# Kernel optimization log

Hardware: AMD Instinct MI355X
Metric: run time of the kernel (lower is better)

Reference implementation:

```python
import jax, jax.numpy as jnp
import numpy as np

H = 56; W = 56; WS = 7; SS = 3; NH = 12; DIM = 384; B = 32
N = WS * WS                      # 49 tokens per window
NW = (H // WS) * (W // WS)       # 64 windows per image
HID = 4 * DIM
EPS = 1e-5


def _rel_index():
    coords = np.stack(np.meshgrid(np.arange(WS), np.arange(WS), indexing='ij'))  # [2,ws,ws]
    cf = coords.reshape(2, -1)
    rel = (cf[:, :, None] - cf[:, None, :]).transpose(1, 2, 0)  # [N,N,2]
    rel[..., 0] += WS - 1
    rel[..., 1] += WS - 1
    rel[..., 0] *= 2 * WS - 1
    return rel.sum(-1).astype(np.int32)  # [N,N] in [0,169)


def _attn_mask():
    img = np.zeros((H, W), np.float32)
    cnt = 0
    sl = (slice(0, -WS), slice(-WS, -SS), slice(-SS, None))
    for h in sl:
        for w in sl:
            img[h, w] = cnt
            cnt += 1
    mw = img.reshape(H // WS, WS, W // WS, WS).transpose(0, 2, 1, 3).reshape(-1, N)  # [nW,N]
    am = mw[:, None, :] - mw[:, :, None]  # [nW,N,N]
    return np.where(am != 0, np.float32(-100.0), np.float32(0.0)).astype(np.float32)


def _ln(x, g, b):
    m = jnp.mean(x, axis=-1, keepdims=True)
    v = jnp.mean(jnp.square(x - m), axis=-1, keepdims=True)
    return (x - m) * jax.lax.rsqrt(v + EPS) * g + b


def setup_inputs() -> dict:
    key = jax.random.key(0)
    ks = jax.random.split(key, 8)
    s = 0.02
    return {
        'x': jax.random.normal(ks[0], (B, H * W, DIM), jnp.float32),
        'qkv_w': jax.random.normal(ks[1], (3 * DIM, DIM), jnp.float32) * s,
        'qkv_b': jnp.zeros((3 * DIM,), jnp.float32),
        'proj_w': jax.random.normal(ks[2], (DIM, DIM), jnp.float32) * s,
        'proj_b': jnp.zeros((DIM,), jnp.float32),
        'rpb_table': jax.random.normal(ks[3], ((2 * WS - 1) ** 2, NH), jnp.float32) * s,
        'ln1_g': jnp.ones((DIM,), jnp.float32),
        'ln1_b': jnp.zeros((DIM,), jnp.float32),
        'fc1_w': jax.random.normal(ks[4], (HID, DIM), jnp.float32) * s,
        'fc1_b': jnp.zeros((HID,), jnp.float32),
        'fc2_w': jax.random.normal(ks[5], (DIM, HID), jnp.float32) * s,
        'fc2_b': jnp.zeros((DIM,), jnp.float32),
        'ln2_g': jnp.ones((DIM,), jnp.float32),
        'ln2_b': jnp.zeros((DIM,), jnp.float32),
        'attn_mask': jnp.asarray(_attn_mask()),
        'rel_idx': jnp.asarray(_rel_index()),
    }


def reference(x, qkv_w, qkv_b, proj_w, proj_b, rpb_table, ln1_g, ln1_b,
              fc1_w, fc1_b, fc2_w, fc2_b, ln2_g, ln2_b, attn_mask, rel_idx):
    Bb, L, C = x.shape
    hd = C // NH
    scale = hd ** -0.5
    shortcut = x
    # cyclic shift
    xs = jnp.roll(x.reshape(Bb, H, W, C), (-SS, -SS), axis=(1, 2))
    # window partition -> [Bb*nW, N, C]
    xw = xs.reshape(Bb, H // WS, WS, W // WS, WS, C).transpose(0, 1, 3, 2, 4, 5).reshape(-1, N, C)
    # qkv
    qkv = (xw @ qkv_w.T + qkv_b).reshape(-1, N, 3, NH, hd).transpose(2, 0, 3, 1, 4)
    q, k, v = qkv[0] * scale, qkv[1], qkv[2]          # [Bb*nW, NH, N, hd]
    attn = jnp.einsum('whnd,whmd->whnm', q, k)        # [Bb*nW, NH, N, N]
    bias = rpb_table[rel_idx.reshape(-1)].reshape(N, N, NH).transpose(2, 0, 1)
    attn = attn + bias[None]
    # shifted-window mask
    attn = attn.reshape(Bb, NW, NH, N, N) + attn_mask[None, :, None]
    attn = jax.nn.softmax(attn.reshape(-1, NH, N, N), axis=-1)
    out = jnp.einsum('whnm,whmd->whnd', attn, v).transpose(0, 2, 1, 3).reshape(-1, N, C)
    out = out @ proj_w.T + proj_b
    # window reverse + roll back
    xs = out.reshape(Bb, H // WS, W // WS, WS, WS, C).transpose(0, 1, 3, 2, 4, 5).reshape(Bb, H, W, C)
    xs = jnp.roll(xs, (SS, SS), axis=(1, 2)).reshape(Bb, L, C)
    # post-norm residuals (as in source: shortcut + norm(attn_out); x += norm(ffn(x)))
    x1 = shortcut + _ln(xs, ln1_g, ln1_b)
    y = jax.nn.gelu(x1 @ fc1_w.T + fc1_b, approximate=False) @ fc2_w.T + fc2_b
    return x1 + _ln(y, ln2_g, ln2_b)
```

## Files before the change

### kernel.cpp

```cpp
#include <hip/hip_runtime.h>
#include <hip/hip_bf16.h>
#include <math.h>

typedef __hip_bfloat16 bf16;
typedef __bf16 bf16x8 __attribute__((ext_vector_type(8)));
typedef float f32x4 __attribute__((ext_vector_type(4)));

#define HH 56
#define WW 56
#define WSZ 7
#define SSH 3
#define NHEAD 12
#define CDIM 384
#define BBATCH 32
#define NTOK 49
#define NWIN 64
#define HIDD 1536
#define HD 32
#define NWTOT (BBATCH*NWIN)
#define MROWS (NWTOT*NTOK)
#define MHALF (MROWS/2)
#define LTOT (HH*WW)
#define EPSLN 1e-5f
#define QSCALE 0.17677669529663687f
#define NEGBIG -1e30f

enum { M_QK = 0, M_V = 1, M_FC1 = 2 };

__device__ __forceinline__ void gload16(const void* g, void* l) {
    __builtin_amdgcn_global_load_lds(
        (const __attribute__((address_space(1))) void*)g,
        (__attribute__((address_space(3))) void*)l, 16, 0, 0);
}

__device__ __forceinline__ unsigned short bfbits(float v) {
    bf16 b = __float2bfloat16(v);
    return *reinterpret_cast<unsigned short*>(&b);
}

__device__ __forceinline__ int xcd_swz(int orig, int nwg) {
    const int q = nwg >> 3, r = nwg & 7;
    const int xcd = orig & 7, loc = orig >> 3;
    return (xcd < r ? xcd * (q + 1) : r * (q + 1) + (xcd - r) * q) + loc;
}

__global__ __launch_bounds__(256) void cvt_k(const float* __restrict__ src,
                                             bf16* __restrict__ dst, int n) {
    int i = blockIdx.x * 256 + threadIdx.x;
    if (i < n) dst[i] = __float2bfloat16(src[i]);
}

__global__ __launch_bounds__(256)
void tbl_k(const float* __restrict__ rpb, const int* __restrict__ relidx,
           const float* __restrict__ amask, float* __restrict__ tbl) {
    int idx = blockIdx.x * 256 + threadIdx.x;
    int m = idx & 63, n = (idx >> 6) & 63;
    int h = (idx >> 12) % NHEAD, wi = idx / (64 * 64 * NHEAD);
    float v;
    if (m >= NTOK) v = NEGBIG;
    else if (n >= NTOK) v = 0.f;
    else v = rpb[relidx[n * NTOK + m] * NHEAD + h] + amask[((long)wi * NTOK + n) * NTOK + m];
    tbl[idx] = v;
}

__global__ __launch_bounds__(256) void gather_k(const float* __restrict__ x,
                                                bf16* __restrict__ xw) {
    int idx = blockIdx.x * 256 + threadIdx.x;
    int rr = idx / 96, c4 = (idx % 96) * 4;
    int w = rr / 49, ti = rr % 49;
    int b = w >> 6, wi = w & 63;
    int hy = (wi >> 3) * 7 + ti / 7;
    int hx = (wi & 7) * 7 + ti % 7;
    int sh = hy + SSH; if (sh >= HH) sh -= HH;
    int sw = hx + SSH; if (sw >= WW) sw -= WW;
    float4 v = *(const float4*)&x[((long)b * LTOT + sh * WW + sw) * CDIM + c4];
    bf16* o = &xw[(long)rr * CDIM + c4];
    o[0] = __float2bfloat16(v.x); o[1] = __float2bfloat16(v.y);
    o[2] = __float2bfloat16(v.z); o[3] = __float2bfloat16(v.w);
}

template<int MODE, int KDIM, int NTN>
__global__ __launch_bounds__(256)
void mgemm_k(const bf16* __restrict__ A, const bf16* __restrict__ Wt,
             const float* __restrict__ bias, void* __restrict__ Outp)
{
    constexpr bool SWAP = (MODE != M_V);
    __shared__ bf16 As[2][128 * 64];
    __shared__ bf16 Bs[2][128 * 64];
    const int tid = threadIdx.x;
    const int wid = tid >> 6, lane = tid & 63;

    const int gid = xcd_swz(blockIdx.x, gridDim.x);
    const int m0 = (gid / NTN) * 128;
    const int n0 = (gid % NTN) * 128;

    const int srow = lane >> 3, sseg = lane & 7;
    const int swseg = sseg ^ (srow & 7);
    const bf16* Ag = A + (long)(m0 + wid * 32 + srow) * KDIM + swseg * 8;
    const bf16* Wg = Wt + (long)(n0 + wid * 32 + srow) * KDIM + swseg * 8;

    const int wr = (wid >> 1) * 64, wc = (wid & 1) * 64;
    const int l15 = lane & 15, g4 = lane >> 4;

    f32x4 acc[4][4] = {};

    auto STAGE = [&](int b, int t) {
#pragma unroll
        for (int i = 0; i < 4; ++i) {
            gload16(Ag + (long)(i * 8) * KDIM + t * 64, &As[b][(wid * 32 + i * 8) * 64]);
            gload16(Wg + (long)(i * 8) * KDIM + t * 64, &Bs[b][(wid * 32 + i * 8) * 64]);
        }
    };

    const int nt = KDIM / 64;
    STAGE(0, 0);
    STAGE(1, 1);
    asm volatile("s_waitcnt vmcnt(8)" ::: "memory");
    __builtin_amdgcn_s_barrier();

    int buf = 0;
    for (int t = 0; t < nt; ++t) {
        bf16x8 af[2][4], bfr[2][4];
#pragma unroll
        for (int kk = 0; kk < 2; ++kk)
#pragma unroll
            for (int i = 0; i < 4; ++i) {
                const int ra = wr + i * 16 + l15;
                const int rb = wc + i * 16 + l15;
                const int sa = (4 * kk + g4) ^ (ra & 7);
                const int sb = (4 * kk + g4) ^ (rb & 7);
                af[kk][i]  = *(const bf16x8*)&As[buf][ra * 64 + sa * 8];
                bfr[kk][i] = *(const bf16x8*)&Bs[buf][rb * 64 + sb * 8];
            }
        __builtin_amdgcn_sched_barrier(0);
        asm volatile("s_waitcnt lgkmcnt(0)" ::: "memory");
        __builtin_amdgcn_sched_barrier(0);
        __builtin_amdgcn_s_barrier();
        if (t + 2 < nt) STAGE(buf, t + 2);
#pragma unroll
        for (int kk = 0; kk < 2; ++kk)
#pragma unroll
            for (int mi = 0; mi < 4; ++mi)
#pragma unroll
                for (int ni = 0; ni < 4; ++ni) {
                    if (SWAP)
                        acc[ni][mi] = __builtin_amdgcn_mfma_f32_16x16x32_bf16(
                            bfr[kk][ni], af[kk][mi], acc[ni][mi], 0, 0, 0);
                    else
                        acc[mi][ni] = __builtin_amdgcn_mfma_f32_16x16x32_bf16(
                            af[kk][mi], bfr[kk][ni], acc[mi][ni], 0, 0, 0);
                }
        if (t + 2 < nt) { asm volatile("s_waitcnt vmcnt(8)" ::: "memory"); }
        else            { asm volatile("s_waitcnt vmcnt(0)" ::: "memory"); }
        __builtin_amdgcn_s_barrier();
        buf ^= 1;
    }

    if (MODE == M_V) {
#pragma unroll
        for (int mi = 0; mi < 4; ++mi) {
            const int mb = m0 + wr + mi * 16 + g4 * 4;
            const int wv_ = mb / 49, ti0 = mb - wv_ * 49;
#pragma unroll
            for (int ni = 0; ni < 4; ++ni) {
                const int n = n0 + wc + ni * 16 + l15;
                const int h = n >> 5, d = n & 31;
                const float bn = bias[n];
                float v4[4];
#pragma unroll
                for (int j = 0; j < 4; ++j) v4[j] = acc[mi][ni][j] + bn;
                if (ti0 <= 45) {
                    ushort4 u = { bfbits(v4[0]), bfbits(v4[1]), bfbits(v4[2]), bfbits(v4[3]) };
                    *(ushort4*)&((bf16*)Outp)[(((long)wv_ * NHEAD + h) * HD + d) * 64 + ti0] = u;
                } else {
#pragma unroll
                    for (int j = 0; j < 4; ++j) {
                        const int m = mb + j;
                        const int w2 = m / 49, ti = m - w2 * 49;
                        ((bf16*)Outp)[(((long)w2 * NHEAD + h) * HD + d) * 64 + ti]
                            = __float2bfloat16(v4[j]);
                    }
                }
            }
        }
    } else {
        long rowbase[4];
        int wq_[4], ti_[4];
#pragma unroll
        for (int mi = 0; mi < 4; ++mi) {
            const int m = m0 + wr + mi * 16 + l15;
            if (MODE == M_QK) { wq_[mi] = m / 49; ti_[mi] = m - wq_[mi] * 49; }
            else rowbase[mi] = (long)m * HIDD;
        }
#pragma unroll
        for (int ni = 0; ni < 4; ++ni) {
            const int nb = n0 + wc + ni * 16 + g4 * 4;
            const float4 bn = *(const float4*)&bias[nb];
            const float bb[4] = { bn.x, bn.y, bn.z, bn.w };
#pragma unroll
            for (int mi = 0; mi < 4; ++mi) {
                float v4[4];
#pragma unroll
                for (int j = 0; j < 4; ++j) v4[j] = acc[ni][mi][j] + bb[j];
                if (MODE == M_FC1) {
#pragma unroll
                    for (int j = 0; j < 4; ++j)
                        v4[j] = 0.5f * v4[j] * (1.0f + erff(v4[j] * 0.70710678118654752f));
                } else {
                    if (nb < CDIM) {
#pragma unroll
                        for (int j = 0; j < 4; ++j) v4[j] *= QSCALE;
                    }
                }
                ushort4 u = { bfbits(v4[0]), bfbits(v4[1]), bfbits(v4[2]), bfbits(v4[3]) };
                if (MODE == M_QK) {
                    const int which = nb >= CDIM;
                    const int hb = (nb - which * CDIM) >> 5, d0 = nb & 31;
                    *(ushort4*)&((bf16*)Outp)[
                        ((((long)wq_[mi] * 2 + which) * NHEAD + hb) * NTOK + ti_[mi]) * HD + d0] = u;
                } else {
                    *(ushort4*)&((bf16*)Outp)[rowbase[mi] + nb] = u;
                }
            }
        }
    }
}

template<int KDIM, bool SCATTER>
__global__ __launch_bounds__(512, 2)
void gemm_ln_k(const bf16* __restrict__ A, const bf16* __restrict__ Wt,
               const float* __restrict__ bias, const float* __restrict__ base,
               const float* __restrict__ lng, const float* __restrict__ lnb,
               float* __restrict__ outp, bf16* __restrict__ outb)
{
    __shared__ bf16 As[2][128 * 64];
    __shared__ bf16 Bs[2][384 * 64];
    const int tid = threadIdx.x;
    const int wid = tid >> 6, lane = tid & 63;

    const int m0 = xcd_swz(blockIdx.x, gridDim.x) * 128;

    const int srow = lane >> 3, sseg = lane & 7;
    const int swseg = sseg ^ (srow & 7);
    const bf16* Ag = A + (long)(m0 + wid * 16 + srow) * KDIM + swseg * 8;
    const bf16* Wg = Wt + (long)(wid * 48 + srow) * KDIM + swseg * 8;

    const int wr = (wid >> 2) * 64, wc = (wid & 3) * 96;
    const int l15 = lane & 15, g4 = lane >> 4;

    f32x4 acc[6][4] = {};

    auto STAGE = [&](int b, int t) {
#pragma unroll
        for (int i = 0; i < 2; ++i)
            gload16(Ag + (long)(i * 8) * KDIM + t * 64, &As[b][(wid * 16 + i * 8) * 64]);
#pragma unroll
        for (int i = 0; i < 6; ++i)
            gload16(Wg + (long)(i * 8) * KDIM + t * 64, &Bs[b][(wid * 48 + i * 8) * 64]);
    };

    const int nt = KDIM / 64;
    STAGE(0, 0);
    STAGE(1, 1);
    asm volatile("s_waitcnt vmcnt(8)" ::: "memory");
    __builtin_amdgcn_s_barrier();

    int buf = 0;
    for (int t = 0; t < nt; ++t) {
        bf16x8 af[2][4], bfr[2][6];
#pragma unroll
        for (int kk = 0; kk < 2; ++kk) {
#pragma unroll
            for (int i = 0; i < 4; ++i) {
                const int ra = wr + i * 16 + l15;
                const int sa = (4 * kk + g4) ^ (ra & 7);
                af[kk][i] = *(const bf16x8*)&As[buf][ra * 64 + sa * 8];
            }
#pragma unroll
            for (int i = 0; i < 6; ++i) {
                const int rb = wc + i * 16 + l15;
                const int sb = (4 * kk + g4) ^ (rb & 7);
                bfr[kk][i] = *(const bf16x8*)&Bs[buf][rb * 64 + sb * 8];
            }
        }
        __builtin_amdgcn_sched_barrier(0);
        asm volatile("s_waitcnt lgkmcnt(0)" ::: "memory");
        __builtin_amdgcn_sched_barrier(0);
        __builtin_amdgcn_s_barrier();
        if (t + 2 < nt) STAGE(buf, t + 2);
#pragma unroll
        for (int kk = 0; kk < 2; ++kk)
#pragma unroll
            for (int ni = 0; ni < 6; ++ni)
#pragma unroll
                for (int mi = 0; mi < 4; ++mi)
                    acc[ni][mi] = __builtin_amdgcn_mfma_f32_16x16x32_bf16(
                        bfr[kk][ni], af[kk][mi], acc[ni][mi], 0, 0, 0);
        if (t + 2 < nt) { asm volatile("s_waitcnt vmcnt(8)" ::: "memory"); }
        else            { asm volatile("s_waitcnt vmcnt(0)" ::: "memory"); }
        __builtin_amdgcn_s_barrier();
        buf ^= 1;
    }

    float psum[4] = {}, psq[4] = {};
#pragma unroll
    for (int ni = 0; ni < 6; ++ni) {
        const int nb = wc + ni * 16 + g4 * 4;
        const float4 bn = *(const float4*)&bias[nb];
        const float bb[4] = { bn.x, bn.y, bn.z, bn.w };
#pragma unroll
        for (int mi = 0; mi < 4; ++mi)
#pragma unroll
            for (int j = 0; j < 4; ++j) {
                float v = acc[ni][mi][j] + bb[j];
                acc[ni][mi][j] = v;
                psum[mi] += v; psq[mi] += v * v;
            }
    }
#pragma unroll
    for (int mi = 0; mi < 4; ++mi) {
        psum[mi] += __shfl_xor(psum[mi], 16); psum[mi] += __shfl_xor(psum[mi], 32);
        psq[mi]  += __shfl_xor(psq[mi], 16);  psq[mi]  += __shfl_xor(psq[mi], 32);
    }
    float* lnp = (float*)&As[0][0];
    const int wcid = wid & 3;
    if (g4 == 0) {
#pragma unroll
        for (int mi = 0; mi < 4; ++mi) {
            const int rl = wr + mi * 16 + l15;
            lnp[wcid * 128 + rl] = psum[mi];
            lnp[512 + wcid * 128 + rl] = psq[mi];
        }
    }
    __syncthreads();

#pragma unroll
    for (int mi = 0; mi < 4; ++mi) {
        const int rl = wr + mi * 16 + l15;
        const float s  = lnp[rl] + lnp[128 + rl] + lnp[256 + rl] + lnp[384 + rl];
        const float sq = lnp[512 + rl] + lnp[640 + rl] + lnp[768 + rl] + lnp[896 + rl];
        const float mean = s * (1.f / 384.f);
        const float rstd = rsqrtf(sq * (1.f / 384.f) - mean * mean + EPSLN);

        const int m = m0 + rl;
        long tok;
        if (SCATTER) {
            int w = m / 49, ti = m - w * 49;
            int b = w >> 6, wi = w & 63;
            int hy = (wi >> 3) * 7 + ti / 7;
            int hx = (wi & 7) * 7 + ti % 7;
            int dh = hy + SSH; if (dh >= HH) dh -= HH;
            int dw = hx + SSH; if (dw >= WW) dw -= WW;
            tok = (long)b * LTOT + dh * WW + dw;
        } else {
            tok = m;
        }
#pragma unroll
        for (int ni = 0; ni < 6; ++ni) {
            const int c = wc + ni * 16 + g4 * 4;
            const float4 gv = *(const float4*)&lng[c];
            const float4 bv = *(const float4*)&lnb[c];
            const float4 xv = *(const float4*)&base[tok * CDIM + c];
            float4 r;
            r.x = xv.x + (acc[ni][mi][0] - mean) * rstd * gv.x + bv.x;
            r.y = xv.y + (acc[ni][mi][1] - mean) * rstd * gv.y + bv.y;
            r.z = xv.z + (acc[ni][mi][2] - mean) * rstd * gv.z + bv.z;
            r.w = xv.w + (acc[ni][mi][3] - mean) * rstd * gv.w + bv.w;
            *(float4*)&outp[tok * CDIM + c] = r;
            if (SCATTER) {
                ushort4 u = { bfbits(r.x), bfbits(r.y), bfbits(r.z), bfbits(r.w) };
                *(ushort4*)&outb[tok * CDIM + c] = u;
            }
        }
    }
}

__global__ __launch_bounds__(256)
void mattn_k(const bf16* __restrict__ qk, const bf16* __restrict__ vT,
             const float* __restrict__ tbl, bf16* __restrict__ attn_out)
{
    __shared__ bf16 Plds[4][64 * 72];
    const int tid = threadIdx.x, wid = tid >> 6, lane = tid & 63;
    const int t = blockIdx.x * 4 + wid;
    const int w = t / NHEAD, h = t % NHEAD, wi = w & 63;
    const int l15 = lane & 15, g = lane >> 4;
    const bf16* qb = qk + ((long)(w * 2 + 0) * NHEAD + h) * (NTOK * HD);
    const bf16* kb = qk + ((long)(w * 2 + 1) * NHEAD + h) * (NTOK * HD);
    const bf16* vt = vT + ((long)w * NHEAD + h) * (HD * 64);
    const float* Tb = tbl + (long)(wi * NHEAD + h) * 64 * 64;
    char* Pw = (char*)&Plds[wid][0];

    bf16x8 kf[4], qf[4];
#pragma unroll
    for (int i = 0; i < 4; ++i) {
        kf[i] = *(const bf16x8*)&kb[(16 * i + l15) * HD + 8 * g];
        qf[i] = *(const bf16x8*)&qb[(16 * i + l15) * HD + 8 * g];
    }
    f32x4 s[4][4] = {};
#pragma unroll
    for (int mi = 0; mi < 4; ++mi)
#pragma unroll
        for (int ni = 0; ni < 4; ++ni)
            s[mi][ni] = __builtin_amdgcn_mfma_f32_16x16x32_bf16(
                kf[mi], qf[ni], s[mi][ni], 0, 0, 0);

#pragma unroll
    for (int ni = 0; ni < 4; ++ni) {
        const int n = 16 * ni + l15;
#pragma unroll
        for (int mi = 0; mi < 4; ++mi) {
            float4 tv = *(const float4*)&Tb[(long)n * 64 + 16 * mi + 4 * g];
            s[mi][ni][0] += tv.x; s[mi][ni][1] += tv.y;
            s[mi][ni][2] += tv.z; s[mi][ni][3] += tv.w;
        }
        float mx = NEGBIG;
#pragma unroll
        for (int mi = 0; mi < 4; ++mi)
#pragma unroll
            for (int j = 0; j < 4; ++j) mx = fmaxf(mx, s[mi][ni][j]);
        mx = fmaxf(mx, __shfl_xor(mx, 16));
        mx = fmaxf(mx, __shfl_xor(mx, 32));
        float sum = 0.f;
#pragma unroll
        for (int mi = 0; mi < 4; ++mi)
#pragma unroll
            for (int j = 0; j < 4; ++j) {
                float e = expf(s[mi][ni][j] - mx);
                s[mi][ni][j] = e; sum += e;
            }
        sum += __shfl_xor(sum, 16);
        sum += __shfl_xor(sum, 32);
        const float r = 1.0f / sum;
#pragma unroll
        for (int mi = 0; mi < 4; ++mi) {
            ushort4 u;
            u.x = bfbits(s[mi][ni][0] * r);
            u.y = bfbits(s[mi][ni][1] * r);
            u.z = bfbits(s[mi][ni][2] * r);
            u.w = bfbits(s[mi][ni][3] * r);
            *(ushort4*)(Pw + (long)n * 144 + (16 * mi + 4 * g) * 2) = u;
        }
    }

    f32x4 o[4][2] = {};
#pragma unroll
    for (int kk = 0; kk < 2; ++kk) {
        bf16x8 vf[2];
        vf[0] = *(const bf16x8*)&vt[(long)(l15) * 64 + 32 * kk + 8 * g];
        vf[1] = *(const bf16x8*)&vt[(long)(16 + l15) * 64 + 32 * kk + 8 * g];
#pragma unroll
        for (int rt = 0; rt < 4; ++rt) {
            bf16x8 pf = *(const bf16x8*)(Pw + (long)(16 * rt + l15) * 144 + (32 * kk + 8 * g) * 2);
            o[rt][0] = __builtin_amdgcn_mfma_f32_16x16x32_bf16(pf, vf[0], o[rt][0], 0, 0, 0);
            o[rt][1] = __builtin_amdgcn_mfma_f32_16x16x32_bf16(pf, vf[1], o[rt][1], 0, 0, 0);
        }
    }

#pragma unroll
    for (int rt = 0; rt < 4; ++rt)
#pragma unroll
        for (int dt = 0; dt < 2; ++dt)
#pragma unroll
            for (int j = 0; j < 4; ++j) {
                int n = 16 * rt + 4 * g + j;
                if (n < NTOK)
                    attn_out[((long)w * NTOK + n) * CDIM + h * HD + 16 * dt + l15]
                        = __float2bfloat16(o[rt][dt][j]);
            }
}

extern "C" void kernel_launch(void* const* d_in, const int* in_sizes, int n_in,
                              void* d_out, int out_size, void* d_ws, size_t ws_size,
                              hipStream_t stream)
{
    const float* x      = (const float*)d_in[0];
    const float* qkv_w  = (const float*)d_in[1];
    const float* qkv_b  = (const float*)d_in[2];
    const float* proj_w = (const float*)d_in[3];
    const float* proj_b = (const float*)d_in[4];
    const float* rpb    = (const float*)d_in[5];
    const float* ln1_g  = (const float*)d_in[6];
    const float* ln1_b  = (const float*)d_in[7];
    const float* fc1_w  = (const float*)d_in[8];
    const float* fc1_b  = (const float*)d_in[9];
    const float* fc2_w  = (const float*)d_in[10];
    const float* fc2_b  = (const float*)d_in[11];
    const float* ln2_g  = (const float*)d_in[12];
    const float* ln2_b  = (const float*)d_in[13];
    const float* amask  = (const float*)d_in[14];
    const int*   relidx = (const int*)d_in[15];
    float* out = (float*)d_out;
    char*  ws  = (char*)d_ws;

    bf16*  wq   = (bf16*) (ws + 0L);
    bf16*  wp   = (bf16*) (ws + 884736L);
    bf16*  w1   = (bf16*) (ws + 1179648L);
    bf16*  w2   = (bf16*) (ws + 2359296L);
    float* tbl  = (float*)(ws + 3538944L);
    bf16*  xw   = (bf16*) (ws + 16121856L);
    bf16*  qkb  = (bf16*) (ws + 93192192L);
    bf16*  vTb  = (bf16*) (ws + 247332864L);
    bf16*  attn_o = (bf16*)(ws + 16121856L);
    bf16*  x1b  = (bf16*) (ws + 93192192L);
    bf16*  H1   = (bf16*) (ws + 170262528L);

    dim3 b256(256), b512(512);

    cvt_k<<<dim3((3*CDIM*CDIM + 255)/256), b256, 0, stream>>>(qkv_w, wq, 3*CDIM*CDIM);
    cvt_k<<<dim3((CDIM*CDIM + 255)/256), b256, 0, stream>>>(proj_w, wp, CDIM*CDIM);
    cvt_k<<<dim3((HIDD*CDIM + 255)/256), b256, 0, stream>>>(fc1_w, w1, HIDD*CDIM);
    cvt_k<<<dim3((CDIM*HIDD + 255)/256), b256, 0, stream>>>(fc2_w, w2, CDIM*HIDD);
    tbl_k<<<dim3(64*12*64*64/256), b256, 0, stream>>>(rpb, relidx, amask, tbl);
    gather_k<<<dim3(MROWS * 96 / 256), b256, 0, stream>>>(x, xw);

    mgemm_k<M_QK, CDIM, 6><<<dim3((MROWS/128)*6), b256, 0, stream>>>(
        xw, wq, qkv_b, (void*)qkb);
    mgemm_k<M_V, CDIM, 3><<<dim3((MROWS/128)*3), b256, 0, stream>>>(
        xw, wq + (long)2*CDIM*CDIM, qkv_b + 2*CDIM, (void*)vTb);

    mattn_k<<<dim3(NWTOT * NHEAD / 4), b256, 0, stream>>>(qkb, vTb, tbl, attn_o);

    gemm_ln_k<CDIM, true><<<dim3(MROWS/128), b512, 0, stream>>>(
        attn_o, wp, proj_b, x, ln1_g, ln1_b, out, x1b);

    for (int c = 0; c < 2; ++c) {
        const long off = (long)c * MHALF * CDIM;
        mgemm_k<M_FC1, CDIM, 12><<<dim3((MHALF/128)*12), b256, 0, stream>>>(
            x1b + off, w1, fc1_b, (void*)H1);
        gemm_ln_k<HIDD, false><<<dim3(MHALF/128), b512, 0, stream>>>(
            H1, w2, fc2_b, out + off, ln2_g, ln2_b, out + off, nullptr);
    }
}
```

Measured before the change: 1.092 ms.

## Load GEMM weight fragments directly from global memory, bypassing LDS

Both GEMM kernels stop staging the weight tile in shared memory and instead read B fragments straight from global memory/L2 into registers. Only the activation tile goes through LDS, with a simpler one-ahead prefetch and __syncthreads. gemm_ln_k moves to 1024 threads with smaller per-wave row tiles and a dedicated LDS buffer for the LayerNorm reductions. The aim is to cut LDS traffic and footprint to raise occupancy, at the risk of exposed global-load latency, poorly coalesced weight reads and tighter register limits.

```diff
diff --git a/kernel.cpp b/kernel.cpp
--- a/kernel.cpp
+++ b/kernel.cpp
@@ -80,13 +80,12 @@
 }
 
 template<int MODE, int KDIM, int NTN>
-__global__ __launch_bounds__(256)
+__global__ __launch_bounds__(256, 4)
 void mgemm_k(const bf16* __restrict__ A, const bf16* __restrict__ Wt,
              const float* __restrict__ bias, void* __restrict__ Outp)
 {
     constexpr bool SWAP = (MODE != M_V);
     __shared__ bf16 As[2][128 * 64];
-    __shared__ bf16 Bs[2][128 * 64];
     const int tid = threadIdx.x;
     const int wid = tid >> 6, lane = tid & 63;
 
@@ -97,62 +96,50 @@
     const int srow = lane >> 3, sseg = lane & 7;
     const int swseg = sseg ^ (srow & 7);
     const bf16* Ag = A + (long)(m0 + wid * 32 + srow) * KDIM + swseg * 8;
-    const bf16* Wg = Wt + (long)(n0 + wid * 32 + srow) * KDIM + swseg * 8;
 
     const int wr = (wid >> 1) * 64, wc = (wid & 1) * 64;
     const int l15 = lane & 15, g4 = lane >> 4;
+    const bf16* Wb = Wt + (long)(n0 + wc + l15) * KDIM + g4 * 8;
 
     f32x4 acc[4][4] = {};
 
     auto STAGE = [&](int b, int t) {
 #pragma unroll
-        for (int i = 0; i < 4; ++i) {
+        for (int i = 0; i < 4; ++i)
             gload16(Ag + (long)(i * 8) * KDIM + t * 64, &As[b][(wid * 32 + i * 8) * 64]);
-            gload16(Wg + (long)(i * 8) * KDIM + t * 64, &Bs[b][(wid * 32 + i * 8) * 64]);
-        }
     };
 
     const int nt = KDIM / 64;
     STAGE(0, 0);
-    STAGE(1, 1);
-    asm volatile("s_waitcnt vmcnt(8)" ::: "memory");
-    __builtin_amdgcn_s_barrier();
-
+    __syncthreads();
     int buf = 0;
     for (int t = 0; t < nt; ++t) {
-        bf16x8 af[2][4], bfr[2][4];
-#pragma unroll
-        for (int kk = 0; kk < 2; ++kk)
+        if (t + 1 < nt) STAGE(buf ^ 1, t + 1);
+#pragma unroll
+        for (int kk = 0; kk < 2; ++kk) {
+            bf16x8 bfr[4], af[4];
+#pragma unroll
+            for (int i = 0; i < 4; ++i)
+                bfr[i] = *(const bf16x8*)&Wb[(long)(i * 16) * KDIM + t * 64 + kk * 32];
 #pragma unroll
             for (int i = 0; i < 4; ++i) {
                 const int ra = wr + i * 16 + l15;
-                const int rb = wc + i * 16 + l15;
                 const int sa = (4 * kk + g4) ^ (ra & 7);
-                const int sb = (4 * kk + g4) ^ (rb & 7);
-                af[kk][i]  = *(const bf16x8*)&As[buf][ra * 64 + sa * 8];
-                bfr[kk][i] = *(const bf16x8*)&Bs[buf][rb * 64 + sb * 8];
-            }
-        __builtin_amdgcn_sched_barrier(0);
-        asm volatile("s_waitcnt lgkmcnt(0)" ::: "memory");
-        __builtin_amdgcn_sched_barrier(0);
-        __builtin_amdgcn_s_barrier();
-        if (t + 2 < nt) STAGE(buf, t + 2);
-#pragma unroll
-        for (int kk = 0; kk < 2; ++kk)
+                af[i] = *(const bf16x8*)&As[buf][ra * 64 + sa * 8];
+            }
 #pragma unroll
             for (int mi = 0; mi < 4; ++mi)
 #pragma unroll
                 for (int ni = 0; ni < 4; ++ni) {
                     if (SWAP)
                         acc[ni][mi] = __builtin_amdgcn_mfma_f32_16x16x32_bf16(
-                            bfr[kk][ni], af[kk][mi], acc[ni][mi], 0, 0, 0);
+                            bfr[ni], af[mi], acc[ni][mi], 0, 0, 0);
                     else
                         acc[mi][ni] = __builtin_amdgcn_mfma_f32_16x16x32_bf16(
-                            af[kk][mi], bfr[kk][ni], acc[mi][ni], 0, 0, 0);
+                            af[mi], bfr[ni], acc[mi][ni], 0, 0, 0);
                 }
-        if (t + 2 < nt) { asm volatile("s_waitcnt vmcnt(8)" ::: "memory"); }
-        else            { asm volatile("s_waitcnt vmcnt(0)" ::: "memory"); }
-        __builtin_amdgcn_s_barrier();
+        }
+        __syncthreads();
         buf ^= 1;
     }
 
@@ -227,14 +214,14 @@
 }
 
 template<int KDIM, bool SCATTER>
-__global__ __launch_bounds__(512, 2)
+__global__ __launch_bounds__(1024, 4)
 void gemm_ln_k(const bf16* __restrict__ A, const bf16* __restrict__ Wt,
                const float* __restrict__ bias, const float* __restrict__ base,
                const float* __restrict__ lng, const float* __restrict__ lnb,
                float* __restrict__ outp, bf16* __restrict__ outb)
 {
     __shared__ bf16 As[2][128 * 64];
-    __shared__ bf16 Bs[2][384 * 64];
+    __shared__ float lnp[1024];
     const int tid = threadIdx.x;
     const int wid = tid >> 6, lane = tid & 63;
 
@@ -242,74 +229,56 @@
 
     const int srow = lane >> 3, sseg = lane & 7;
     const int swseg = sseg ^ (srow & 7);
-    const bf16* Ag = A + (long)(m0 + wid * 16 + srow) * KDIM + swseg * 8;
-    const bf16* Wg = Wt + (long)(wid * 48 + srow) * KDIM + swseg * 8;
-
-    const int wr = (wid >> 2) * 64, wc = (wid & 3) * 96;
+    const bf16* Ag = A + (long)(m0 + wid * 8 + srow) * KDIM + swseg * 8;
+
+    const int wm = wid >> 2, wn = wid & 3;
+    const int wr = wm * 32, wc = wn * 96;
     const int l15 = lane & 15, g4 = lane >> 4;
-
-    f32x4 acc[6][4] = {};
+    const bf16* Wb = Wt + (long)(wc + l15) * KDIM + g4 * 8;
+
+    f32x4 acc[6][2] = {};
 
     auto STAGE = [&](int b, int t) {
-#pragma unroll
-        for (int i = 0; i < 2; ++i)
-            gload16(Ag + (long)(i * 8) * KDIM + t * 64, &As[b][(wid * 16 + i * 8) * 64]);
-#pragma unroll
-        for (int i = 0; i < 6; ++i)
-            gload16(Wg + (long)(i * 8) * KDIM + t * 64, &Bs[b][(wid * 48 + i * 8) * 64]);
+        gload16(Ag + t * 64, &As[b][(wid * 8) * 64]);
     };
 
     const int nt = KDIM / 64;
     STAGE(0, 0);
-    STAGE(1, 1);
-    asm volatile("s_waitcnt vmcnt(8)" ::: "memory");
-    __builtin_amdgcn_s_barrier();
-
+    __syncthreads();
     int buf = 0;
     for (int t = 0; t < nt; ++t) {
-        bf16x8 af[2][4], bfr[2][6];
+        if (t + 1 < nt) STAGE(buf ^ 1, t + 1);
 #pragma unroll
         for (int kk = 0; kk < 2; ++kk) {
-#pragma unroll
-            for (int i = 0; i < 4; ++i) {
+            bf16x8 bfr[6], af[2];
+#pragma unroll
+            for (int i = 0; i < 6; ++i)
+                bfr[i] = *(const bf16x8*)&Wb[(long)(i * 16) * KDIM + t * 64 + kk * 32];
+#pragma unroll
+            for (int i = 0; i < 2; ++i) {
                 const int ra = wr + i * 16 + l15;
                 const int sa = (4 * kk + g4) ^ (ra & 7);
-                af[kk][i] = *(const bf16x8*)&As[buf][ra * 64 + sa * 8];
-            }
-#pragma unroll
-            for (int i = 0; i < 6; ++i) {
-                const int rb = wc + i * 16 + l15;
-                const int sb = (4 * kk + g4) ^ (rb & 7);
-                bfr[kk][i] = *(const bf16x8*)&Bs[buf][rb * 64 + sb * 8];
-            }
-        }
-        __builtin_amdgcn_sched_barrier(0);
-        asm volatile("s_waitcnt lgkmcnt(0)" ::: "memory");
-        __builtin_amdgcn_sched_barrier(0);
-        __builtin_amdgcn_s_barrier();
-        if (t + 2 < nt) STAGE(buf, t + 2);
-#pragma unroll
-        for (int kk = 0; kk < 2; ++kk)
+                af[i] = *(const bf16x8*)&As[buf][ra * 64 + sa * 8];
+            }
 #pragma unroll
             for (int ni = 0; ni < 6; ++ni)
 #pragma unroll
-                for (int mi = 0; mi < 4; ++mi)
+                for (int mi = 0; mi < 2; ++mi)
                     acc[ni][mi] = __builtin_amdgcn_mfma_f32_16x16x32_bf16(
-                        bfr[kk][ni], af[kk][mi], acc[ni][mi], 0, 0, 0);
-        if (t + 2 < nt) { asm volatile("s_waitcnt vmcnt(8)" ::: "memory"); }
-        else            { asm volatile("s_waitcnt vmcnt(0)" ::: "memory"); }
-        __builtin_amdgcn_s_barrier();
+                        bfr[ni], af[mi], acc[ni][mi], 0, 0, 0);
+        }
+        __syncthreads();
         buf ^= 1;
     }
 
-    float psum[4] = {}, psq[4] = {};
+    float psum[2] = {}, psq[2] = {};
 #pragma unroll
     for (int ni = 0; ni < 6; ++ni) {
         const int nb = wc + ni * 16 + g4 * 4;
         const float4 bn = *(const float4*)&bias[nb];
         const float bb[4] = { bn.x, bn.y, bn.z, bn.w };
 #pragma unroll
-        for (int mi = 0; mi < 4; ++mi)
+        for (int mi = 0; mi < 2; ++mi)
 #pragma unroll
             for (int j = 0; j < 4; ++j) {
                 float v = acc[ni][mi][j] + bb[j];
@@ -318,24 +287,22 @@
             }
     }
 #pragma unroll
-    for (int mi = 0; mi < 4; ++mi) {
+    for (int mi = 0; mi < 2; ++mi) {
         psum[mi] += __shfl_xor(psum[mi], 16); psum[mi] += __shfl_xor(psum[mi], 32);
         psq[mi]  += __shfl_xor(psq[mi], 16);  psq[mi]  += __shfl_xor(psq[mi], 32);
     }
-    float* lnp = (float*)&As[0][0];
-    const int wcid = wid & 3;
     if (g4 == 0) {
 #pragma unroll
-        for (int mi = 0; mi < 4; ++mi) {
+        for (int mi = 0; mi < 2; ++mi) {
             const int rl = wr + mi * 16 + l15;
-            lnp[wcid * 128 + rl] = psum[mi];
-            lnp[512 + wcid * 128 + rl] = psq[mi];
+            lnp[wn * 128 + rl] = psum[mi];
+            lnp[512 + wn * 128 + rl] = psq[mi];
         }
     }
     __syncthreads();
 
 #pragma unroll
-    for (int mi = 0; mi < 4; ++mi) {
+    for (int mi = 0; mi < 2; ++mi) {
         const int rl = wr + mi * 16 + l15;
         const float s  = lnp[rl] + lnp[128 + rl] + lnp[256 + rl] + lnp[384 + rl];
         const float sq = lnp[512 + rl] + lnp[640 + rl] + lnp[768 + rl] + lnp[896 + rl];
@@ -504,7 +471,7 @@
     bf16*  x1b  = (bf16*) (ws + 93192192L);
     bf16*  H1   = (bf16*) (ws + 170262528L);
 
-    dim3 b256(256), b512(512);
+    dim3 b256(256), b1024(1024);
 
     cvt_k<<<dim3((3*CDIM*CDIM + 255)/256), b256, 0, stream>>>(qkv_w, wq, 3*CDIM*CDIM);
     cvt_k<<<dim3((CDIM*CDIM + 255)/256), b256, 0, stream>>>(proj_w, wp, CDIM*CDIM);
@@ -520,14 +487,14 @@
 
     mattn_k<<<dim3(NWTOT * NHEAD / 4), b256, 0, stream>>>(qkb, vTb, tbl, attn_o);
 
-    gemm_ln_k<CDIM, true><<<dim3(MROWS/128), b512, 0, stream>>>(
+    gemm_ln_k<CDIM, true><<<dim3(MROWS/128), b1024, 0, stream>>>(
         attn_o, wp, proj_b, x, ln1_g, ln1_b, out, x1b);
 
     for (int c = 0; c < 2; ++c) {
         const long off = (long)c * MHALF * CDIM;
         mgemm_k<M_FC1, CDIM, 12><<<dim3((MHALF/128)*12), b256, 0, stream>>>(
             x1b + off, w1, fc1_b, (void*)H1);
-        gemm_ln_k<HIDD, false><<<dim3(MHALF/128), b512, 0, stream>>>(
+        gemm_ln_k<HIDD, false><<<dim3(MHALF/128), b1024, 0, stream>>>(
             H1, w2, fc2_b, out + off, ln2_g, ln2_b, out + off, nullptr);
     }
 }
```

After: 1.635 ms. +49.7%, slower.
